# Performance work log

Measured on AMD Instinct MI355X. Metric: run time of the kernel, lower is better.

## Reference

```python
import jax, jax.numpy as jnp
import numpy as np

B, C1, C2, K, S, P, D, HDIM, BINS = 4, 32, 64, 3, 1, 1, 1, 64, 16
H = W = 96

def _unfold(x):
    # torch F.unfold: (B, C*k*k, L) with channel-major (c, kh, kw) ordering,
    # which matches conv_general_dilated_patches' output feature ordering.
    p = jax.lax.conv_general_dilated_patches(
        x, filter_shape=(K, K), window_strides=(S, S),
        padding=((P, P), (P, P)), rhs_dilation=(D, D))  # (B, C*k*k, Ho, Wo)
    b, ckk, ho, wo = p.shape
    return p.reshape(b, ckk, ho * wo), ho, wo

def _patch_stats(patches):
    # patches: (B, Ckk, L); stop-gradient stats [mu, sigma, gamma, kappa, entropy]
    b, ckk, L = patches.shape
    mu = patches.mean(axis=1, keepdims=True)
    diff = patches - mu
    var = (diff * diff).mean(axis=1, keepdims=True)
    sigma = jnp.sqrt(var + 1e-6)
    z = diff / (sigma + 1e-6)
    gamma = (z ** 3).mean(axis=1, keepdims=True)
    kappa = (z ** 4).mean(axis=1, keepdims=True) - 3.0
    p_min = patches.min(axis=1, keepdims=True)
    p_max = patches.max(axis=1, keepdims=True)
    p_norm = (patches - p_min) / (p_max - p_min + 1e-6)
    bin_idx = jnp.clip((p_norm * (BINS - 1)).astype(jnp.int32), 0, BINS - 1)
    # histogram via flat scatter-add: counts[b, bin, l]
    b_ix = jnp.arange(b, dtype=jnp.int32)[:, None, None]
    l_ix = jnp.arange(L, dtype=jnp.int32)[None, None, :]
    flat = ((b_ix * BINS + bin_idx) * L + l_ix).ravel()
    counts = jnp.zeros(b * BINS * L, dtype=patches.dtype).at[flat].add(1.0)
    counts = counts.reshape(b, BINS, L)
    prob = counts / (ckk + 1e-6)
    entropy = -(prob * jnp.log(prob + 1e-9)).sum(axis=1, keepdims=True)
    stats = jnp.concatenate([mu, sigma, gamma, kappa, entropy], axis=1)  # (B,5,L)
    return jax.lax.stop_gradient(stats)

def setup_inputs() -> dict:
    key = jax.random.key(0)
    ks = jax.random.split(key, 8)
    x = jax.random.normal(ks[0], (B, C1, H, W), dtype=jnp.float32)
    fc1_w = jax.random.normal(ks[1], (HDIM, 5), dtype=jnp.float32) / np.sqrt(5.0)
    fc1_b = jax.random.normal(ks[2], (HDIM,), dtype=jnp.float32) * 0.01
    alpha_w = jax.random.normal(ks[3], (C2, HDIM), dtype=jnp.float32) * 0.01
    alpha_b = jnp.ones((C2,), dtype=jnp.float32)
    phi_w = jax.random.normal(ks[4], (C1 * K * K, HDIM), dtype=jnp.float32) * 0.01
    phi_b = jnp.zeros((C1 * K * K,), dtype=jnp.float32)
    bn_gamma = jnp.ones((C2,), dtype=jnp.float32)
    bn_beta = jnp.zeros((C2,), dtype=jnp.float32)
    bn_mean = jax.random.normal(ks[5], (C2,), dtype=jnp.float32) * 0.1
    bn_var = jax.random.uniform(ks[6], (C2,), dtype=jnp.float32, minval=0.5, maxval=1.5)
    return {"x": x, "fc1_w": fc1_w, "fc1_b": fc1_b, "alpha_w": alpha_w,
            "alpha_b": alpha_b, "phi_w": phi_w, "phi_b": phi_b,
            "bn_gamma": bn_gamma, "bn_beta": bn_beta,
            "bn_mean": bn_mean, "bn_var": bn_var}

def reference(x, fc1_w, fc1_b, alpha_w, alpha_b, phi_w, phi_b,
              bn_gamma, bn_beta, bn_mean, bn_var):
    patches, ho, wo = _unfold(x)           # (B, C1*K*K, L)
    b, ckk, L = patches.shape
    stats = _patch_stats(patches)          # (B, 5, L), stop-grad
    s = stats.transpose(0, 2, 1).reshape(b * L, 5)
    h = jax.nn.relu(s @ fc1_w.T + fc1_b)                 # (B*L, HDIM)
    alpha = (h @ alpha_w.T + alpha_b).reshape(b, L, C2)  # (B, L, C2)
    phi = (h @ phi_w.T + phi_b).reshape(b, L, ckk)       # (B, L, Ckk)
    # kernel = alpha[:,None] * phi[None,:]; out = kernel @ patch
    # == alpha * (phi . patch), computed without materializing kernels
    proj = jnp.einsum('blj,bjl->bl', phi, patches)       # (B, L)
    out = alpha * proj[:, :, None]                       # (B, L, C2)
    out = out.transpose(0, 2, 1).reshape(b, C2, ho, wo)
    # BatchNorm2d (eval: running stats) + SiLU
    inv = bn_gamma / jnp.sqrt(bn_var + 1e-5)
    y = (out - bn_mean[None, :, None, None]) * inv[None, :, None, None] \
        + bn_beta[None, :, None, None]
    return jax.nn.silu(y)
```

## Files before the change

### kernel.cpp

```cpp
#include <hip/hip_runtime.h>

#define FLT_MAX_ 3.402823466e+38f

constexpr int HW   = 9216;
constexpr int AOFF = 4608;
constexpr int CST  = 105;
constexpr int XSW  = 32 * CST;

using bf16x8 = __attribute__((ext_vector_type(8))) short;
using f32x4  = __attribute__((ext_vector_type(4))) float;
using u32x4  = __attribute__((ext_vector_type(4))) unsigned int;

__device__ inline unsigned cvtpk_bf16(float a, float b) {
    unsigned r;
    asm("v_cvt_pk_bf16_f32 %0, %1, %2" : "=v"(r) : "v"(a), "v"(b));
    return r;
}
__device__ inline void split2(float p0, float p1, unsigned &h, unsigned &l) {
    h = cvtpk_bf16(p0, p1);
    const float h0 = __builtin_bit_cast(float, h << 16);
    const float h1 = __builtin_bit_cast(float, h & 0xFFFF0000u);
    l = cvtpk_bf16(p0 - h0, p1 - h1);
}

__global__ __launch_bounds__(256)
void prep_w(const float* __restrict__ phi_w, const float* __restrict__ alpha_w,
            u32x4* __restrict__ wsq) {
    const int kb   = blockIdx.x;
    const int n    = threadIdx.x >> 6;
    const int lane = threadIdx.x & 63;
    const int lg   = lane >> 4, kk = lane & 15;
    if (kb < 9) {
        float p[8];
        #pragma unroll
        for (int jj = 0; jj < 8; ++jj) {
            const int ch = lg * 8 + jj;
            p[jj] = phi_w[(ch * 9 + kb) * 64 + n * 16 + kk];
        }
        unsigned h0,h1,h2,h3, l0,l1,l2,l3;
        split2(p[0],p[1],h0,l0); split2(p[2],p[3],h1,l1);
        split2(p[4],p[5],h2,l2); split2(p[6],p[7],h3,l3);
        wsq[(kb * 4 + n) * 64 + lane]        = u32x4{h0,h1,h2,h3};
        wsq[2304 + (kb * 4 + n) * 64 + lane] = u32x4{l0,l1,l2,l3};
    } else {
        #pragma unroll
        for (int kblk = 0; kblk < 2; ++kblk) {
            float p[8];
            #pragma unroll
            for (int jj = 0; jj < 8; ++jj) {
                const int k = kblk * 32 + lg * 8 + jj;
                p[jj] = alpha_w[(n * 16 + kk) * 64 + k];
            }
            unsigned h0,h1,h2,h3, l0,l1,l2,l3;
            split2(p[0],p[1],h0,l0); split2(p[2],p[3],h1,l1);
            split2(p[4],p[5],h2,l2); split2(p[6],p[7],h3,l3);
            wsq[AOFF + (kblk * 4 + n) * 64 + lane]       = u32x4{h0,h1,h2,h3};
            wsq[AOFF + 512 + (kblk * 4 + n) * 64 + lane] = u32x4{l0,l1,l2,l3};
        }
    }
}

__global__ __launch_bounds__(256)
void sac_fused(const float* __restrict__ x,
               const float* __restrict__ fc1_w, const float* __restrict__ fc1_b,
               const float* __restrict__ alpha_b,
               const float* __restrict__ phi_b,
               const float* __restrict__ bn_g, const float* __restrict__ bn_b,
               const float* __restrict__ bn_m, const float* __restrict__ bn_v,
               const u32x4* __restrict__ wsq,
               float* __restrict__ out)
{
    __shared__ unsigned xs[XSW];
    __shared__ float    h_lds[32 * 65];
    __shared__ unsigned cnts[16 * 132];
    __shared__ float    phib[32];
    __shared__ float    redP[64];

    const int tid  = threadIdx.x;
    const int lane = tid & 63;
    const int w    = __builtin_amdgcn_readfirstlane(tid >> 6);
    const int g    = blockIdx.x;
    const int b    = g / 288;
    const int rem  = g - b * 288;
    const int y0   = rem / 3;
    const int x0   = (rem - y0 * 3) * 32;

    const int p8   = lane & 7;
    const int cg   = lane >> 3;
    const int pos  = w * 8 + p8;
    const int cgh  = cg >> 1;
    const int mycol = pos * 4 + cgh;

    const float* __restrict__ xb = x + (size_t)b * 32 * HW;

    #pragma unroll
    for (int i = 0; i < 14; ++i) {
        const int idx = tid + i * 256;
        if (idx < XSW) {
            const int ch = idx / CST;
            const int rm = idx - ch * CST;
            const int r2 = rm / 35;
            const int c2 = rm - r2 * 35;
            const int y  = y0 + r2 - 1;
            const int xg = x0 + c2 - 1;
            float p = 0.f;
            if ((unsigned)y < 96u && (unsigned)xg < 96u)
                p = xb[ch * HW + y * 96 + xg];
            const unsigned t  = cvtpk_bf16(p, p);
            const float    hf = __builtin_bit_cast(float, t << 16);
            xs[idx] = cvtpk_bf16(p - hf, p);
        }
    }
    #pragma unroll
    for (int bi = 0; bi < 16; ++bi) cnts[bi * 132 + mycol] = 0u;
    __syncthreads();

    float s1 = 0.f, s2 = 0.f, s3 = 0.f, s4 = 0.f;
    float mn = FLT_MAX_, mx = -FLT_MAX_, pj = 0.f;
    {
        const unsigned* __restrict__ xsc = xs + (cg * 4) * CST;
        #pragma unroll
        for (int cc = 0; cc < 4; ++cc)
            #pragma unroll
            for (int dy = 0; dy < 3; ++dy)
                #pragma unroll
                for (int dx = 0; dx < 3; ++dx) {
                    const unsigned Wd = xsc[cc * CST + dy * 35 + pos + dx];
                    const float hf = __builtin_bit_cast(float, Wd & 0xFFFF0000u);
                    const float lf = __builtin_bit_cast(float, Wd << 16);
                    const float p  = hf + lf;
                    const float pp = p * p;
                    s1 += p;
                    s2 = fmaf(p, p, s2);
                    s3 = fmaf(pp, p, s3);
                    s4 = fmaf(pp, pp, s4);
                    mn = fminf(mn, p);
                    mx = fmaxf(mx, p);
                    pj = fmaf(p, phi_b[(cg * 4 + cc) * 9 + dy * 3 + dx], pj);
                }
    }
    #pragma unroll
    for (int msk = 8; msk < 64; msk <<= 1) {
        s1 += __shfl_xor(s1, msk);
        s2 += __shfl_xor(s2, msk);
        s3 += __shfl_xor(s3, msk);
        s4 += __shfl_xor(s4, msk);
        mn = fminf(mn, __shfl_xor(mn, msk));
        mx = fmaxf(mx, __shfl_xor(mx, msk));
        pj += __shfl_xor(pj, msk);
    }
    if (cg == 0) phib[pos] = pj;

    const float mu   = s1 * (1.0f / 288.0f);
    const float rng  = (mx - mn) + 1e-6f;
    const float invr = 1.0f / rng;

    {
        const unsigned* __restrict__ xsc = xs + (cg * 4) * CST;
        #pragma unroll
        for (int cc = 0; cc < 4; ++cc)
            #pragma unroll
            for (int dy = 0; dy < 3; ++dy)
                #pragma unroll
                for (int dx = 0; dx < 3; ++dx) {
                    const unsigned Wd = xsc[cc * CST + dy * 35 + pos + dx];
                    const float hf = __builtin_bit_cast(float, Wd & 0xFFFF0000u);
                    const float lf = __builtin_bit_cast(float, Wd << 16);
                    const float p  = hf + lf;
                    const float pn = (p - mn) * invr;
                    int bi = (int)(pn * 15.0f);
                    bi = bi < 0 ? 0 : (bi > 15 ? 15 : bi);
                    atomicAdd(&cnts[bi * 132 + mycol], 1u);
                }
    }
    asm volatile("s_waitcnt lgkmcnt(0)" ::: "memory");

    float ent = 0.f;
    #pragma unroll
    for (int e = 0; e < 2; ++e) {
        const int bi = cg * 2 + e;
        const unsigned cnt = cnts[bi * 132 + pos * 4 + 0] + cnts[bi * 132 + pos * 4 + 1]
                           + cnts[bi * 132 + pos * 4 + 2] + cnts[bi * 132 + pos * 4 + 3];
        const float prob = (float)cnt * (1.0f / 288.0f);
        ent -= prob * __logf(prob + 1e-9f);
    }
    #pragma unroll
    for (int msk = 8; msk < 64; msk <<= 1) ent += __shfl_xor(ent, msk);

    {
        const float e2  = s2 * (1.0f / 288.0f);
        const float e3  = s3 * (1.0f / 288.0f);
        const float e4  = s4 * (1.0f / 288.0f);
        const float mu2 = mu * mu;
        const float var = fmaxf(e2 - mu2, 0.f);
        const float m3  = e3 - 3.f * mu * e2 + 2.f * mu * mu2;
        const float m4  = e4 - 4.f * mu * e3 + 6.f * mu2 * e2 - 3.f * mu2 * mu2;
        const float sig = sqrtf(var + 1e-6f);
        const float inv = 1.0f / (sig + 1e-6f);
        const float inv2 = inv * inv;
        const float gam = m3 * (inv2 * inv);
        const float kap = m4 * (inv2 * inv2) - 3.0f;
        #pragma unroll
        for (int kk2 = 0; kk2 < 8; ++kk2) {
            const int k = cg * 8 + kk2;
            float acc = fc1_b[k];
            acc = fmaf(mu,  fc1_w[k * 5 + 0], acc);
            acc = fmaf(sig, fc1_w[k * 5 + 1], acc);
            acc = fmaf(gam, fc1_w[k * 5 + 2], acc);
            acc = fmaf(kap, fc1_w[k * 5 + 3], acc);
            acc = fmaf(ent, fc1_w[k * 5 + 4], acc);
            h_lds[pos * 65 + k] = fmaxf(acc, 0.f);
        }
    }
    __syncthreads();

    const int m  = w >> 1;
    const int np = (w & 1) * 2;
    const int lg = lane >> 4;
    const int kk = lane & 15;

    {
        const int acol = m * 16 + kk;
        const unsigned* __restrict__ xsg = xs + (lg * 8) * CST;

        f32x4 acc0 = {0.f, 0.f, 0.f, 0.f};
        f32x4 acc1 = {0.f, 0.f, 0.f, 0.f};

        u32x4 nbh0 = wsq[(0 * 4 + np) * 64 + lane];
        u32x4 nbh1 = wsq[(0 * 4 + np + 1) * 64 + lane];
        u32x4 nbl0 = wsq[2304 + (0 * 4 + np) * 64 + lane];
        u32x4 nbl1 = wsq[2304 + (0 * 4 + np + 1) * 64 + lane];

        #pragma unroll
        for (int tap = 0; tap < 9; ++tap) {
            const int dy = tap / 3, dx = tap % 3;
            const u32x4 bh0 = nbh0, bh1 = nbh1, bl0 = nbl0, bl1 = nbl1;
            if (tap < 8) {
                nbh0 = wsq[((tap + 1) * 4 + np) * 64 + lane];
                nbh1 = wsq[((tap + 1) * 4 + np + 1) * 64 + lane];
                nbl0 = wsq[2304 + ((tap + 1) * 4 + np) * 64 + lane];
                nbl1 = wsq[2304 + ((tap + 1) * 4 + np + 1) * 64 + lane];
            }
            const int abase = dy * 35 + acol + dx;
            const unsigned W0 = xsg[0 * CST + abase], W1 = xsg[1 * CST + abase];
            const unsigned W2 = xsg[2 * CST + abase], W3 = xsg[3 * CST + abase];
            const unsigned W4 = xsg[4 * CST + abase], W5 = xsg[5 * CST + abase];
            const unsigned W6 = xsg[6 * CST + abase], W7 = xsg[7 * CST + abase];
            const unsigned ah0 = __builtin_amdgcn_perm(W1, W0, 0x07060302u);
            const unsigned ah1 = __builtin_amdgcn_perm(W3, W2, 0x07060302u);
            const unsigned ah2 = __builtin_amdgcn_perm(W5, W4, 0x07060302u);
            const unsigned ah3 = __builtin_amdgcn_perm(W7, W6, 0x07060302u);
            const unsigned al0 = __builtin_amdgcn_perm(W1, W0, 0x05040100u);
            const unsigned al1 = __builtin_amdgcn_perm(W3, W2, 0x05040100u);
            const unsigned al2 = __builtin_amdgcn_perm(W5, W4, 0x05040100u);
            const unsigned al3 = __builtin_amdgcn_perm(W7, W6, 0x05040100u);
            const bf16x8 Ah  = __builtin_bit_cast(bf16x8, u32x4{ah0,ah1,ah2,ah3});
            const bf16x8 Al  = __builtin_bit_cast(bf16x8, u32x4{al0,al1,al2,al3});
            const bf16x8 Bh0 = __builtin_bit_cast(bf16x8, bh0);
            const bf16x8 Bl0 = __builtin_bit_cast(bf16x8, bl0);
            const bf16x8 Bh1 = __builtin_bit_cast(bf16x8, bh1);
            const bf16x8 Bl1 = __builtin_bit_cast(bf16x8, bl1);

            acc0 = __builtin_amdgcn_mfma_f32_16x16x32_bf16(Ah, Bh0, acc0, 0, 0, 0);
            acc0 = __builtin_amdgcn_mfma_f32_16x16x32_bf16(Ah, Bl0, acc0, 0, 0, 0);
            acc0 = __builtin_amdgcn_mfma_f32_16x16x32_bf16(Al, Bh0, acc0, 0, 0, 0);
            acc1 = __builtin_amdgcn_mfma_f32_16x16x32_bf16(Ah, Bh1, acc1, 0, 0, 0);
            acc1 = __builtin_amdgcn_mfma_f32_16x16x32_bf16(Ah, Bl1, acc1, 0, 0, 0);
            acc1 = __builtin_amdgcn_mfma_f32_16x16x32_bf16(Al, Bh1, acc1, 0, 0, 0);
        }

        const int k0 = np * 16 + kk;
        const int k1 = k0 + 16;
        const int pbr = (m * 16 + lg * 4) * 65;
        float pr0 = acc0[0] * h_lds[pbr + 0 * 65 + k0] + acc1[0] * h_lds[pbr + 0 * 65 + k1];
        float pr1 = acc0[1] * h_lds[pbr + 1 * 65 + k0] + acc1[1] * h_lds[pbr + 1 * 65 + k1];
        float pr2 = acc0[2] * h_lds[pbr + 2 * 65 + k0] + acc1[2] * h_lds[pbr + 2 * 65 + k1];
        float pr3 = acc0[3] * h_lds[pbr + 3 * 65 + k0] + acc1[3] * h_lds[pbr + 3 * 65 + k1];
        #pragma unroll
        for (int msk = 1; msk < 16; msk <<= 1) {
            pr0 += __shfl_xor(pr0, msk);
            pr1 += __shfl_xor(pr1, msk);
            pr2 += __shfl_xor(pr2, msk);
            pr3 += __shfl_xor(pr3, msk);
        }
        if (kk == 0) {
            const int pb = m * 16 + lg * 4;
            redP[(pb + 0) * 2 + (w & 1)] = pr0;
            redP[(pb + 1) * 2 + (w & 1)] = pr1;
            redP[(pb + 2) * 2 + (w & 1)] = pr2;
            redP[(pb + 3) * 2 + (w & 1)] = pr3;
        }
    }
    __syncthreads();

    const int pb4 = m * 16 + lg * 4;
    const float pj0 = redP[(pb4 + 0) * 2] + redP[(pb4 + 0) * 2 + 1] + phib[pb4 + 0];
    const float pj1 = redP[(pb4 + 1) * 2] + redP[(pb4 + 1) * 2 + 1] + phib[pb4 + 1];
    const float pj2 = redP[(pb4 + 2) * 2] + redP[(pb4 + 2) * 2 + 1] + phib[pb4 + 2];
    const float pj3 = redP[(pb4 + 3) * 2] + redP[(pb4 + 3) * 2 + 1] + phib[pb4 + 3];

    f32x4 ac0 = {0.f, 0.f, 0.f, 0.f};
    f32x4 ac1 = {0.f, 0.f, 0.f, 0.f};
    #pragma unroll
    for (int kblk = 0; kblk < 2; ++kblk) {
        const float* hp = &h_lds[(m * 16 + kk) * 65 + kblk * 32 + lg * 8];
        const float h0 = hp[0], h1 = hp[1], h2 = hp[2], h3 = hp[3];
        const float h4 = hp[4], h5 = hp[5], h6 = hp[6], h7 = hp[7];
        unsigned ah0,ah1,ah2,ah3, al0,al1,al2,al3;
        split2(h0,h1,ah0,al0); split2(h2,h3,ah1,al1);
        split2(h4,h5,ah2,al2); split2(h6,h7,ah3,al3);
        const bf16x8 Ah = __builtin_bit_cast(bf16x8, u32x4{ah0,ah1,ah2,ah3});
        const bf16x8 Al = __builtin_bit_cast(bf16x8, u32x4{al0,al1,al2,al3});
        const u32x4 bh0 = wsq[AOFF + (kblk * 4 + np) * 64 + lane];
        const u32x4 bh1 = wsq[AOFF + (kblk * 4 + np + 1) * 64 + lane];
        const u32x4 bl0 = wsq[AOFF + 512 + (kblk * 4 + np) * 64 + lane];
        const u32x4 bl1 = wsq[AOFF + 512 + (kblk * 4 + np + 1) * 64 + lane];
        const bf16x8 Bh0 = __builtin_bit_cast(bf16x8, bh0);
        const bf16x8 Bl0 = __builtin_bit_cast(bf16x8, bl0);
        const bf16x8 Bh1 = __builtin_bit_cast(bf16x8, bh1);
        const bf16x8 Bl1 = __builtin_bit_cast(bf16x8, bl1);
        ac0 = __builtin_amdgcn_mfma_f32_16x16x32_bf16(Ah, Bh0, ac0, 0, 0, 0);
        ac0 = __builtin_amdgcn_mfma_f32_16x16x32_bf16(Ah, Bl0, ac0, 0, 0, 0);
        ac0 = __builtin_amdgcn_mfma_f32_16x16x32_bf16(Al, Bh0, ac0, 0, 0, 0);
        ac1 = __builtin_amdgcn_mfma_f32_16x16x32_bf16(Ah, Bh1, ac1, 0, 0, 0);
        ac1 = __builtin_amdgcn_mfma_f32_16x16x32_bf16(Ah, Bl1, ac1, 0, 0, 0);
        ac1 = __builtin_amdgcn_mfma_f32_16x16x32_bf16(Al, Bh1, ac1, 0, 0, 0);
    }

    const int c0 = np * 16 + kk;
    const size_t obase = (size_t)(b * 64) * HW + (size_t)y0 * 96 + x0 + m * 16 + lg * 4;
    {
        const int ch     = c0;
        const float ab_  = alpha_b[ch];
        const float binv = bn_g[ch] * rsqrtf(bn_v[ch] + 1e-5f);
        const float bm_  = bn_m[ch], bb_ = bn_b[ch];
        const float o0 = (ac0[0] + ab_) * pj0, o1 = (ac0[1] + ab_) * pj1;
        const float o2 = (ac0[2] + ab_) * pj2, o3 = (ac0[3] + ab_) * pj3;
        const float y0v = (o0 - bm_) * binv + bb_;
        const float y1v = (o1 - bm_) * binv + bb_;
        const float y2v = (o2 - bm_) * binv + bb_;
        const float y3v = (o3 - bm_) * binv + bb_;
        f32x4 sv;
        sv[0] = __fdividef(y0v, 1.0f + __expf(-y0v));
        sv[1] = __fdividef(y1v, 1.0f + __expf(-y1v));
        sv[2] = __fdividef(y2v, 1.0f + __expf(-y2v));
        sv[3] = __fdividef(y3v, 1.0f + __expf(-y3v));
        *(f32x4*)&out[obase + (size_t)ch * HW] = sv;
    }
    {
        const int ch     = c0 + 16;
        const float ab_  = alpha_b[ch];
        const float binv = bn_g[ch] * rsqrtf(bn_v[ch] + 1e-5f);
        const float bm_  = bn_m[ch], bb_ = bn_b[ch];
        const float o0 = (ac1[0] + ab_) * pj0, o1 = (ac1[1] + ab_) * pj1;
        const float o2 = (ac1[2] + ab_) * pj2, o3 = (ac1[3] + ab_) * pj3;
        const float y0v = (o0 - bm_) * binv + bb_;
        const float y1v = (o1 - bm_) * binv + bb_;
        const float y2v = (o2 - bm_) * binv + bb_;
        const float y3v = (o3 - bm_) * binv + bb_;
        f32x4 sv;
        sv[0] = __fdividef(y0v, 1.0f + __expf(-y0v));
        sv[1] = __fdividef(y1v, 1.0f + __expf(-y1v));
        sv[2] = __fdividef(y2v, 1.0f + __expf(-y2v));
        sv[3] = __fdividef(y3v, 1.0f + __expf(-y3v));
        *(f32x4*)&out[obase + (size_t)ch * HW] = sv;
    }
}

extern "C" void kernel_launch(void* const* d_in, const int* in_sizes, int n_in,
                              void* d_out, int out_size, void* d_ws, size_t ws_size,
                              hipStream_t stream) {
    const float* x   = (const float*)d_in[0];
    const float* f1w = (const float*)d_in[1];
    const float* f1b = (const float*)d_in[2];
    const float* aw  = (const float*)d_in[3];
    const float* ab  = (const float*)d_in[4];
    const float* pw  = (const float*)d_in[5];
    const float* pb  = (const float*)d_in[6];
    const float* bg  = (const float*)d_in[7];
    const float* bb  = (const float*)d_in[8];
    const float* bm  = (const float*)d_in[9];
    const float* bv  = (const float*)d_in[10];

    u32x4* wsq = (u32x4*)d_ws;

    prep_w<<<dim3(10), dim3(256), 0, stream>>>(pw, aw, wsq);
    sac_fused<<<dim3(1152), dim3(256), 0, stream>>>(
        x, f1w, f1b, ab, pb, bg, bb, bm, bv, wsq, (float*)d_out);
}
```

Measured before the change: 32.51 us.

## Reorganize LDS tile to cell-major swizzled layout with vectorized reads and register reuse

Changes the shared-memory input tile from channel-major to cell-major with an XOR-swizzled channel grouping, so each thread reads four or eight channels of a cell with one 128-bit LDS load instead of scalar loads. Pixel words are cached in registers between the stats pass and the histogram pass, which removes the second LDS read sweep and drops the bin clamp. Also prefetches the alpha weights before the barrier and adds a launch-bounds occupancy hint. The extra cached registers may raise register pressure, and removing the clamp relies on the normalized value staying within range.

Measured after the change: 30.59 us. 5.9% less time.

```diff
diff --git a/kernel.cpp b/kernel.cpp
--- a/kernel.cpp
+++ b/kernel.cpp
@@ -2,10 +2,12 @@
 
 #define FLT_MAX_ 3.402823466e+38f
 
-constexpr int HW   = 9216;
-constexpr int AOFF = 4608;
-constexpr int CST  = 105;
-constexpr int XSW  = 32 * CST;
+constexpr int HW    = 9216;
+constexpr int AOFF  = 4608;
+constexpr int CW    = 34;
+constexpr int NCELL = 3 * CW;
+constexpr int CSTR  = 36;
+constexpr int XSW   = NCELL * CSTR;
 
 using bf16x8 = __attribute__((ext_vector_type(8))) short;
 using f32x4  = __attribute__((ext_vector_type(4))) float;
@@ -60,7 +62,7 @@
     }
 }
 
-__global__ __launch_bounds__(256)
+__global__ __launch_bounds__(256, 4)
 void sac_fused(const float* __restrict__ x,
                const float* __restrict__ fc1_w, const float* __restrict__ fc1_b,
                const float* __restrict__ alpha_b,
@@ -85,22 +87,21 @@
     const int y0   = rem / 3;
     const int x0   = (rem - y0 * 3) * 32;
 
-    const int p8   = lane & 7;
-    const int cg   = lane >> 3;
-    const int pos  = w * 8 + p8;
-    const int cgh  = cg >> 1;
-    const int mycol = pos * 4 + cgh;
+    const int p8    = lane & 7;
+    const int cg    = lane >> 3;
+    const int pos   = w * 8 + p8;
+    const int mycol = pos * 4 + (cg >> 1);
 
     const float* __restrict__ xb = x + (size_t)b * 32 * HW;
 
     #pragma unroll
-    for (int i = 0; i < 14; ++i) {
+    for (int i = 0; i < 13; ++i) {
         const int idx = tid + i * 256;
-        if (idx < XSW) {
-            const int ch = idx / CST;
-            const int rm = idx - ch * CST;
-            const int r2 = rm / 35;
-            const int c2 = rm - r2 * 35;
+        if (idx < 32 * NCELL) {
+            const int ch = idx / NCELL;
+            const int rm = idx - ch * NCELL;
+            const int r2 = rm / CW;
+            const int c2 = rm - r2 * CW;
             const int y  = y0 + r2 - 1;
             const int xg = x0 + c2 - 1;
             float p = 0.f;
@@ -108,37 +109,43 @@
                 p = xb[ch * HW + y * 96 + xg];
             const unsigned t  = cvtpk_bf16(p, p);
             const float    hf = __builtin_bit_cast(float, t << 16);
-            xs[idx] = cvtpk_bf16(p - hf, p);
+            const int cell = rm;
+            const int word = cell * CSTR + ((((ch >> 3) ^ (cell & 3)) << 3) | (ch & 7));
+            xs[word] = cvtpk_bf16(p - hf, p);
         }
     }
     #pragma unroll
     for (int bi = 0; bi < 16; ++bi) cnts[bi * 132 + mycol] = 0u;
     __syncthreads();
 
+    u32x4 pw4[9];
     float s1 = 0.f, s2 = 0.f, s3 = 0.f, s4 = 0.f;
     float mn = FLT_MAX_, mx = -FLT_MAX_, pj = 0.f;
-    {
-        const unsigned* __restrict__ xsc = xs + (cg * 4) * CST;
-        #pragma unroll
-        for (int cc = 0; cc < 4; ++cc)
+    #pragma unroll
+    for (int dy = 0; dy < 3; ++dy)
+        #pragma unroll
+        for (int dx = 0; dx < 3; ++dx) {
+            const int tap  = dy * 3 + dx;
+            const int cell = dy * CW + pos + dx;
+            const int base = cell * CSTR + ((((cg >> 1) ^ (cell & 3)) << 3) | ((cg & 1) << 2));
+            const u32x4 w4 = *(const u32x4*)&xs[base];
+            pw4[tap] = w4;
             #pragma unroll
-            for (int dy = 0; dy < 3; ++dy)
-                #pragma unroll
-                for (int dx = 0; dx < 3; ++dx) {
-                    const unsigned Wd = xsc[cc * CST + dy * 35 + pos + dx];
-                    const float hf = __builtin_bit_cast(float, Wd & 0xFFFF0000u);
-                    const float lf = __builtin_bit_cast(float, Wd << 16);
-                    const float p  = hf + lf;
-                    const float pp = p * p;
-                    s1 += p;
-                    s2 = fmaf(p, p, s2);
-                    s3 = fmaf(pp, p, s3);
-                    s4 = fmaf(pp, pp, s4);
-                    mn = fminf(mn, p);
-                    mx = fmaxf(mx, p);
-                    pj = fmaf(p, phi_b[(cg * 4 + cc) * 9 + dy * 3 + dx], pj);
-                }
-    }
+            for (int cc = 0; cc < 4; ++cc) {
+                const unsigned u = w4[cc];
+                const float hf = __builtin_bit_cast(float, u & 0xFFFF0000u);
+                const float lf = __builtin_bit_cast(float, u << 16);
+                const float p  = hf + lf;
+                const float pp = p * p;
+                s1 += p;
+                s2 = fmaf(p, p, s2);
+                s3 = fmaf(pp, p, s3);
+                s4 = fmaf(pp, pp, s4);
+                mn = fminf(mn, p);
+                mx = fmaxf(mx, p);
+                pj = fmaf(p, phi_b[(cg * 4 + cc) * 9 + tap], pj);
+            }
+        }
     #pragma unroll
     for (int msk = 8; msk < 64; msk <<= 1) {
         s1 += __shfl_xor(s1, msk);
@@ -155,23 +162,19 @@
     const float rng  = (mx - mn) + 1e-6f;
     const float invr = 1.0f / rng;
 
-    {
-        const unsigned* __restrict__ xsc = xs + (cg * 4) * CST;
-        #pragma unroll
-        for (int cc = 0; cc < 4; ++cc)
-            #pragma unroll
-            for (int dy = 0; dy < 3; ++dy)
-                #pragma unroll
-                for (int dx = 0; dx < 3; ++dx) {
-                    const unsigned Wd = xsc[cc * CST + dy * 35 + pos + dx];
-                    const float hf = __builtin_bit_cast(float, Wd & 0xFFFF0000u);
-                    const float lf = __builtin_bit_cast(float, Wd << 16);
-                    const float p  = hf + lf;
-                    const float pn = (p - mn) * invr;
-                    int bi = (int)(pn * 15.0f);
-                    bi = bi < 0 ? 0 : (bi > 15 ? 15 : bi);
-                    atomicAdd(&cnts[bi * 132 + mycol], 1u);
-                }
+    #pragma unroll
+    for (int tap = 0; tap < 9; ++tap) {
+        const u32x4 w4 = pw4[tap];
+        #pragma unroll
+        for (int cc = 0; cc < 4; ++cc) {
+            const unsigned u = w4[cc];
+            const float hf = __builtin_bit_cast(float, u & 0xFFFF0000u);
+            const float lf = __builtin_bit_cast(float, u << 16);
+            const float p  = hf + lf;
+            const float pn = (p - mn) * invr;
+            const int  bi  = (int)(pn * 15.0f);
+            atomicAdd(&cnts[bi * 132 + mycol], 1u);
+        }
     }
     asm volatile("s_waitcnt lgkmcnt(0)" ::: "memory");
 
@@ -221,7 +224,6 @@
 
     {
         const int acol = m * 16 + kk;
-        const unsigned* __restrict__ xsg = xs + (lg * 8) * CST;
 
         f32x4 acc0 = {0.f, 0.f, 0.f, 0.f};
         f32x4 acc1 = {0.f, 0.f, 0.f, 0.f};
@@ -241,19 +243,18 @@
                 nbl0 = wsq[2304 + ((tap + 1) * 4 + np) * 64 + lane];
                 nbl1 = wsq[2304 + ((tap + 1) * 4 + np + 1) * 64 + lane];
             }
-            const int abase = dy * 35 + acol + dx;
-            const unsigned W0 = xsg[0 * CST + abase], W1 = xsg[1 * CST + abase];
-            const unsigned W2 = xsg[2 * CST + abase], W3 = xsg[3 * CST + abase];
-            const unsigned W4 = xsg[4 * CST + abase], W5 = xsg[5 * CST + abase];
-            const unsigned W6 = xsg[6 * CST + abase], W7 = xsg[7 * CST + abase];
-            const unsigned ah0 = __builtin_amdgcn_perm(W1, W0, 0x07060302u);
-            const unsigned ah1 = __builtin_amdgcn_perm(W3, W2, 0x07060302u);
-            const unsigned ah2 = __builtin_amdgcn_perm(W5, W4, 0x07060302u);
-            const unsigned ah3 = __builtin_amdgcn_perm(W7, W6, 0x07060302u);
-            const unsigned al0 = __builtin_amdgcn_perm(W1, W0, 0x05040100u);
-            const unsigned al1 = __builtin_amdgcn_perm(W3, W2, 0x05040100u);
-            const unsigned al2 = __builtin_amdgcn_perm(W5, W4, 0x05040100u);
-            const unsigned al3 = __builtin_amdgcn_perm(W7, W6, 0x05040100u);
+            const int cell = dy * CW + acol + dx;
+            const int base = cell * CSTR + (((lg ^ (cell & 3))) << 3);
+            const u32x4 W03 = *(const u32x4*)&xs[base];
+            const u32x4 W47 = *(const u32x4*)&xs[base + 4];
+            const unsigned ah0 = __builtin_amdgcn_perm(W03[1], W03[0], 0x07060302u);
+            const unsigned ah1 = __builtin_amdgcn_perm(W03[3], W03[2], 0x07060302u);
+            const unsigned ah2 = __builtin_amdgcn_perm(W47[1], W47[0], 0x07060302u);
+            const unsigned ah3 = __builtin_amdgcn_perm(W47[3], W47[2], 0x07060302u);
+            const unsigned al0 = __builtin_amdgcn_perm(W03[1], W03[0], 0x05040100u);
+            const unsigned al1 = __builtin_amdgcn_perm(W03[3], W03[2], 0x05040100u);
+            const unsigned al2 = __builtin_amdgcn_perm(W47[1], W47[0], 0x05040100u);
+            const unsigned al3 = __builtin_amdgcn_perm(W47[3], W47[2], 0x05040100u);
             const bf16x8 Ah  = __builtin_bit_cast(bf16x8, u32x4{ah0,ah1,ah2,ah3});
             const bf16x8 Al  = __builtin_bit_cast(bf16x8, u32x4{al0,al1,al2,al3});
             const bf16x8 Bh0 = __builtin_bit_cast(bf16x8, bh0);
@@ -291,6 +292,15 @@
             redP[(pb + 3) * 2 + (w & 1)] = pr3;
         }
     }
+
+    const u32x4 Abh0_0 = wsq[AOFF + (0 * 4 + np) * 64 + lane];
+    const u32x4 Abh1_0 = wsq[AOFF + (0 * 4 + np + 1) * 64 + lane];
+    const u32x4 Abl0_0 = wsq[AOFF + 512 + (0 * 4 + np) * 64 + lane];
+    const u32x4 Abl1_0 = wsq[AOFF + 512 + (0 * 4 + np + 1) * 64 + lane];
+    const u32x4 Abh0_1 = wsq[AOFF + (1 * 4 + np) * 64 + lane];
+    const u32x4 Abh1_1 = wsq[AOFF + (1 * 4 + np + 1) * 64 + lane];
+    const u32x4 Abl0_1 = wsq[AOFF + 512 + (1 * 4 + np) * 64 + lane];
+    const u32x4 Abl1_1 = wsq[AOFF + 512 + (1 * 4 + np + 1) * 64 + lane];
     __syncthreads();
 
     const int pb4 = m * 16 + lg * 4;
@@ -311,14 +321,10 @@
         split2(h4,h5,ah2,al2); split2(h6,h7,ah3,al3);
         const bf16x8 Ah = __builtin_bit_cast(bf16x8, u32x4{ah0,ah1,ah2,ah3});
         const bf16x8 Al = __builtin_bit_cast(bf16x8, u32x4{al0,al1,al2,al3});
-        const u32x4 bh0 = wsq[AOFF + (kblk * 4 + np) * 64 + lane];
-        const u32x4 bh1 = wsq[AOFF + (kblk * 4 + np + 1) * 64 + lane];
-        const u32x4 bl0 = wsq[AOFF + 512 + (kblk * 4 + np) * 64 + lane];
-        const u32x4 bl1 = wsq[AOFF + 512 + (kblk * 4 + np + 1) * 64 + lane];
-        const bf16x8 Bh0 = __builtin_bit_cast(bf16x8, bh0);
-        const bf16x8 Bl0 = __builtin_bit_cast(bf16x8, bl0);
-        const bf16x8 Bh1 = __builtin_bit_cast(bf16x8, bh1);
-        const bf16x8 Bl1 = __builtin_bit_cast(bf16x8, bl1);
+        const bf16x8 Bh0 = __builtin_bit_cast(bf16x8, kblk == 0 ? Abh0_0 : Abh0_1);
+        const bf16x8 Bl0 = __builtin_bit_cast(bf16x8, kblk == 0 ? Abl0_0 : Abl0_1);
+        const bf16x8 Bh1 = __builtin_bit_cast(bf16x8, kblk == 0 ? Abh1_0 : Abh1_1);
+        const bf16x8 Bl1 = __builtin_bit_cast(bf16x8, kblk == 0 ? Abl1_0 : Abl1_1);
         ac0 = __builtin_amdgcn_mfma_f32_16x16x32_bf16(Ah, Bh0, ac0, 0, 0, 0);
         ac0 = __builtin_amdgcn_mfma_f32_16x16x32_bf16(Ah, Bl0, ac0, 0, 0, 0);
         ac0 = __builtin_amdgcn_mfma_f32_16x16x32_bf16(Al, Bh0, ac0, 0, 0, 0);
```
